# Optimization experiments

Hardware: AMD Instinct MI355X
Metric: run time of the kernel (lower is better)

## Reference

```python
import jax, jax.numpy as jnp
import numpy as np

B, C, D, H, W = 1, 64, 24, 24, 24
N = D * H * W
K = D + H + W - 2  # cross neighbors per node (self deduped)
DS, GD = 64, 64    # d_sim, g_dim
GROUPS = C // 4
EPS = 1e-5
N_ITERS = 2        # pool_strides = [1, 1]


def _build_nbr_idx():
    i, j, k = np.meshgrid(np.arange(D), np.arange(H), np.arange(W), indexing='ij')
    i, j, k = i.reshape(-1), j.reshape(-1), k.reshape(-1)
    a0 = (j * W + k)[:, None] + np.arange(D)[None, :] * (H * W)      # (N, D) full depth line (incl self)
    full1 = (i * H * W + k)[:, None] + np.arange(H)[None, :] * W     # (N, H)
    a1 = full1[np.arange(H)[None, :] != j[:, None]].reshape(N, H - 1)
    full2 = (i * H * W + j * W)[:, None] + np.arange(W)[None, :]     # (N, W)
    a2 = full2[np.arange(W)[None, :] != k[:, None]].reshape(N, W - 1)
    return np.concatenate([a0, a1, a2], axis=1).astype(np.int32)     # (N, K)


def setup_inputs() -> dict:
    key = jax.random.key(0)
    ks = jax.random.split(key, 8)
    s = 0.05
    return {
        'x': jax.random.normal(ks[0], (B, C, D, H, W), jnp.float32),
        'nbr_idx': jnp.asarray(_build_nbr_idx()),
        'phi_w': jax.random.normal(ks[1], (DS, C), jnp.float32) * s,
        'phi_b': jnp.zeros((DS,), jnp.float32),
        'theta_w': jax.random.normal(ks[2], (DS, C), jnp.float32) * s,
        'theta_b': jnp.zeros((DS,), jnp.float32),
        'G_w': jax.random.normal(ks[3], (GD, C), jnp.float32) * s,
        'G_b': jnp.zeros((GD,), jnp.float32),
        'r_w': jax.random.normal(ks[4], (C, GD), jnp.float32) * s,
        'r_b': jnp.zeros((C,), jnp.float32),
        'gn_gamma': jnp.ones((N_ITERS, C), jnp.float32),
        'gn_beta': jnp.zeros((N_ITERS, C), jnp.float32),
        'bn_gamma': jnp.ones((C,), jnp.float32),
        'bn_beta': jnp.zeros((C,), jnp.float32),
        'bn_mean': jnp.zeros((C,), jnp.float32),
        'bn_var': jnp.ones((C,), jnp.float32),
    }


def _group_norm(v, gamma, beta):
    vg = v.reshape(B, GROUPS, C // GROUPS, D, H, W)
    m = vg.mean(axis=(2, 3, 4, 5), keepdims=True)
    var = ((vg - m) ** 2).mean(axis=(2, 3, 4, 5), keepdims=True)
    vn = ((vg - m) / jnp.sqrt(var + EPS)).reshape(B, C, D, H, W)
    return vn * gamma[None, :, None, None, None] + beta[None, :, None, None, None]


def reference(x, nbr_idx, phi_w, phi_b, theta_w, theta_b, G_w, G_b, r_w, r_b,
              gn_gamma, gn_beta, bn_gamma, bn_beta, bn_mean, bn_var):
    h = x
    for it in range(N_ITERS):
        hf = h.reshape(B, C, N).transpose(2, 0, 1)                    # (N, B, C) node features
        theta = jnp.einsum('nbc,dc->nbd', hf, theta_w) + theta_b     # (N, B, DS) queries
        phi_all = jnp.einsum('nbc,dc->nbd', hf, phi_w) + phi_b       # (N, B, DS) keys (pre-gather)
        g_all = jnp.einsum('nbc,gc->nbg', hf, G_w) + G_b             # (N, B, GD) values (pre-gather)
        phi_e = phi_all[nbr_idx]                                      # (N, K, B, DS) mailbox gather
        g_e = g_all[nbr_idx]                                          # (N, K, B, GD)
        f = jnp.einsum('nbd,nkbd->nbk', theta, phi_e)                # attention logits over K
        a = jax.nn.softmax(f, axis=-1)                                # non_local_merge 'softmax'
        y = jnp.einsum('nbk,nkbg->nbg', a, g_e)                      # weighted value sum
        cross = jnp.einsum('nbg,cg->nbc', y, r_w) + r_b              # (N, B, C) output proj
        cross = cross.transpose(1, 2, 0).reshape(B, C, D, H, W)
        h = h + _group_norm(cross, gn_gamma[it], gn_beta[it])
    # BatchNorm3d (eval, running stats) + ReLU
    bc = lambda v: v[None, :, None, None, None]
    out = (h - bc(bn_mean)) / jnp.sqrt(bc(bn_var) + EPS) * bc(bn_gamma) + bc(bn_beta)
    return jax.nn.relu(out)
```

## Files before the change

### kernel.cpp

```cpp
#include <hip/hip_runtime.h>
#include <math.h>

#define NN 13824
#define LW 24

__global__ __launch_bounds__(256) void apply_proj_kernel(
    const float* __restrict__ x,
    const float* __restrict__ cross, const float* __restrict__ gsum,
    const float* __restrict__ gn_g, const float* __restrict__ gn_b,
    float* __restrict__ h_out, int mode,
    const float* __restrict__ theta_w, const float* __restrict__ theta_b,
    const float* __restrict__ phi_w, const float* __restrict__ phi_b,
    const float* __restrict__ g_w, const float* __restrict__ g_b,
    float* __restrict__ tpg)
{
    __shared__ float hs[64 * 64];
    __shared__ float ws[64 * 68];

    const int tid = threadIdx.x;
    const int tile = blockIdx.x / 3, ts = blockIdx.x % 3;
    const int n0 = tile * 64;

    const float* wsel = (ts == 0) ? theta_w : (ts == 1) ? phi_w : g_w;
    const float* bsel = (ts == 0) ? theta_b : (ts == 1) ? phi_b : g_b;

    if (mode == 0) {
        for (int i = tid; i < 4096; i += 256) {
            int c = i >> 6, nl = i & 63;
            hs[c * 64 + nl] = x[(size_t)c * NN + n0 + nl];
        }
    } else {
        for (int i = tid; i < 4096; i += 256) {
            int nl = i >> 6, c = i & 63;
            ws[c * 68 + nl] = cross[(size_t)(n0 + nl) * 64 + c];
        }
        __syncthreads();
        const float inv_cnt = 1.f / 55296.f;
        for (int i = tid; i < 4096; i += 256) {
            int c = i >> 6, nl = i & 63;
            int gr = c >> 2;
            float mean = gsum[gr * 16] * inv_cnt;
            float var = gsum[512 + gr * 16] * inv_cnt - mean * mean;
            float v = (ws[c * 68 + nl] - mean) * rsqrtf(var + 1e-5f) * gn_g[c] + gn_b[c];
            size_t o = (size_t)c * NN + n0 + nl;
            float hv = x[o] + v;
            hs[c * 64 + nl] = hv;
            if (ts == 0) h_out[o] = hv;
        }
        __syncthreads();
    }

    for (int i = tid; i < 4096; i += 256) {
        int d = i >> 6, c = i & 63;
        ws[c * 68 + d] = wsel[d * 64 + c];
    }
    __syncthreads();

    const int d0  = (tid & 15) * 4;
    const int nl0 = (tid >> 4) * 4;
    float acc[4][4];
    #pragma unroll
    for (int q = 0; q < 4; q++)
        #pragma unroll
        for (int j = 0; j < 4; j++) acc[q][j] = 0.f;

    #pragma unroll 4
    for (int c = 0; c < 64; c++) {
        float4 hv = *(const float4*)&hs[c * 64 + nl0];
        float4 wv = *(const float4*)&ws[c * 68 + d0];
        #pragma unroll
        for (int j = 0; j < 4; j++) {
            float w = (&wv.x)[j];
            acc[0][j] += hv.x * w;
            acc[1][j] += hv.y * w;
            acc[2][j] += hv.z * w;
            acc[3][j] += hv.w * w;
        }
    }
    float4 bias = *(const float4*)&bsel[d0];
    #pragma unroll
    for (int q = 0; q < 4; q++) {
        float4 v;
        v.x = acc[q][0] + bias.x; v.y = acc[q][1] + bias.y;
        v.z = acc[q][2] + bias.z; v.w = acc[q][3] + bias.w;
        *(float4*)&tpg[(size_t)(n0 + nl0 + q) * 192 + ts * 64 + d0] = v;
    }
}

__global__ __launch_bounds__(256, 4) void line_attn_kernel(
    const float* __restrict__ tpg,
    float* __restrict__ y_part,
    float* __restrict__ l_part,
    float* __restrict__ gsum)
{
    __shared__ float wbuf[4][2304];

    const int tid = threadIdx.x;
    const int wv = tid >> 6, lane = tid & 63;
    const int line = blockIdx.x * 4 + wv;
    const int axis = line / 576, L = line % 576;
    float* gb = wbuf[wv];
    float* P  = wbuf[wv] + 1632;

    if (blockIdx.x == 0) {
        for (int i = tid; i < 1024; i += 256) gsum[i] = 0.f;
    }

    int base, stride;
    if (axis == 0)      { base = L * 24;                    stride = 1;   }
    else if (axis == 1) { base = (L / 24) * 576 + (L % 24); stride = 24;  }
    else                { base = L;                         stride = 576; }
    const bool excl = (axis != 2);

    float4 gpre[6];
    const int grow = lane >> 4, gquad = lane & 15;
    #pragma unroll
    for (int q = 0; q < 6; q++) {
        int row = q * 4 + grow;
        gpre[q] = *(const float4*)&tpg[(size_t)(base + row * stride) * 192 + 128 + gquad * 4];
    }

    const int li = lane >> 3, lj = lane & 7;
    const int r0 = li * 3, c0 = lj * 3;
    const float* trow[3];
    const float* prow[3];
    #pragma unroll
    for (int a = 0; a < 3; a++) {
        trow[a] = tpg + (size_t)(base + (r0 + a) * stride) * 192;
        prow[a] = tpg + (size_t)(base + (c0 + a) * stride) * 192 + 64;
    }
    float sa[3][3];
    #pragma unroll
    for (int a = 0; a < 3; a++)
        #pragma unroll
        for (int b = 0; b < 3; b++) sa[a][b] = 0.f;
    #pragma unroll 4
    for (int d4 = 0; d4 < 64; d4 += 4) {
        float4 t[3], p[3];
        #pragma unroll
        for (int a = 0; a < 3; a++) t[a] = *(const float4*)&trow[a][d4];
        #pragma unroll
        for (int b = 0; b < 3; b++) p[b] = *(const float4*)&prow[b][d4];
        #pragma unroll
        for (int a = 0; a < 3; a++)
            #pragma unroll
            for (int b = 0; b < 3; b++)
                sa[a][b] += t[a].x * p[b].x + t[a].y * p[b].y +
                            t[a].z * p[b].z + t[a].w * p[b].w;
    }

    float rs[3] = {0.f, 0.f, 0.f};
    #pragma unroll
    for (int a = 0; a < 3; a++)
        #pragma unroll
        for (int b = 0; b < 3; b++) {
            float e = (excl && (r0 + a) == (c0 + b)) ? 0.f : __expf(sa[a][b]);
            rs[a] += e;
            P[(r0 + a) * 28 + c0 + b] = e;
        }
    #pragma unroll
    for (int off = 1; off <= 4; off <<= 1)
        #pragma unroll
        for (int a = 0; a < 3; a++) rs[a] += __shfl_xor(rs[a], off);
    if (lj == 0) {
        #pragma unroll
        for (int a = 0; a < 3; a++)
            l_part[(size_t)axis * NN + base + (r0 + a) * stride] = rs[a];
    }

    #pragma unroll
    for (int q = 0; q < 6; q++)
        *(float4*)&gb[(q * 4 + grow) * 68 + gquad * 4] = gpre[q];
    __threadfence_block();

    const int rg = lane >> 4, dg = lane & 15;
    float acc[6][4];
    #pragma unroll
    for (int i = 0; i < 6; i++)
        #pragma unroll
        for (int k = 0; k < 4; k++) acc[i][k] = 0.f;
    #pragma unroll 4
    for (int c = 0; c < 24; c++) {
        float4 gv = *(const float4*)&gb[c * 68 + dg * 4];
        #pragma unroll
        for (int i = 0; i < 6; i++) {
            float p = P[(rg * 6 + i) * 28 + c];
            acc[i][0] += p * gv.x; acc[i][1] += p * gv.y;
            acc[i][2] += p * gv.z; acc[i][3] += p * gv.w;
        }
    }
    float* yp = y_part + (size_t)axis * NN * 64;
    #pragma unroll
    for (int i = 0; i < 6; i++) {
        float4 v = {acc[i][0], acc[i][1], acc[i][2], acc[i][3]};
        *(float4*)&yp[(size_t)(base + (rg * 6 + i) * stride) * 64 + dg * 4] = v;
    }
}

__global__ __launch_bounds__(256) void combine_kernel(
    const float* __restrict__ y_part, const float* __restrict__ l_part,
    const float* __restrict__ r_w, const float* __restrict__ r_b,
    float* __restrict__ cross, float* __restrict__ gsum)
{
    __shared__ float ys[16 * 68];
    __shared__ float red_s[4][64], red_ss[4][64];

    const int tid = threadIdx.x;
    const int d = tid & 63, w = tid >> 6;
    const int n0 = blockIdx.x * 16;
    const size_t S = (size_t)NN * 64;

    #pragma unroll
    for (int q = 0; q < 4; q++) {
        int nn = w * 4 + q;
        int n = n0 + nn;
        float lv = l_part[n] + l_part[NN + n] + l_part[2 * NN + n];
        size_t o = (size_t)n * 64 + d;
        float yv = y_part[o] + y_part[S + o] + y_part[2 * S + o];
        ys[nn * 68 + d] = yv / lv;
    }
    __syncthreads();

    const int c = d;
    float rb = r_b[c];
    float acc[4] = {rb, rb, rb, rb};
    for (int dd = 0; dd < 64; dd += 4) {
        float4 r4 = *(const float4*)&r_w[c * 64 + dd];
        #pragma unroll
        for (int q = 0; q < 4; q++) {
            float4 y4 = *(const float4*)&ys[(w * 4 + q) * 68 + dd];
            acc[q] += r4.x * y4.x + r4.y * y4.y + r4.z * y4.z + r4.w * y4.w;
        }
    }
    float s = 0.f, ss = 0.f;
    #pragma unroll
    for (int q = 0; q < 4; q++) {
        int n = n0 + w * 4 + q;
        cross[(size_t)n * 64 + c] = acc[q];
        s += acc[q];
        ss += acc[q] * acc[q];
    }
    red_s[w][c] = s;
    red_ss[w][c] = ss;
    __syncthreads();
    if (w == 0) {
        float ts  = red_s[0][c] + red_s[1][c] + red_s[2][c] + red_s[3][c];
        float tss = red_ss[0][c] + red_ss[1][c] + red_ss[2][c] + red_ss[3][c];
        ts  += __shfl_xor(ts, 1);  ts  += __shfl_xor(ts, 2);
        tss += __shfl_xor(tss, 1); tss += __shfl_xor(tss, 2);
        if ((c & 3) == 0) {
            atomicAdd(&gsum[(c >> 2) * 16], ts);
            atomicAdd(&gsum[512 + (c >> 2) * 16], tss);
        }
    }
}

__global__ __launch_bounds__(256) void final_kernel(
    const float* __restrict__ cross,
    const float* __restrict__ gsum,
    const float* __restrict__ gn_g, const float* __restrict__ gn_b,
    const float* __restrict__ h_in,
    const float* __restrict__ bn_g, const float* __restrict__ bn_b,
    const float* __restrict__ bn_m, const float* __restrict__ bn_v,
    float* __restrict__ out)
{
    __shared__ float t[64 * 65];
    const int tid = threadIdx.x;
    const int n0 = blockIdx.x * 64;
    for (int i = tid; i < 4096; i += 256) {
        int nl = i >> 6, c = i & 63;
        t[c * 65 + nl] = cross[(size_t)(n0 + nl) * 64 + c];
    }
    __syncthreads();
    const float inv_cnt = 1.f / 55296.f;
    for (int i = tid; i < 4096; i += 256) {
        int c = i >> 6, nl = i & 63;
        int gr = c >> 2;
        float mean = gsum[gr * 16] * inv_cnt;
        float var = gsum[512 + gr * 16] * inv_cnt - mean * mean;
        float v = (t[c * 65 + nl] - mean) * rsqrtf(var + 1e-5f) * gn_g[c] + gn_b[c];
        size_t o = (size_t)c * NN + n0 + nl;
        float h2 = h_in[o] + v;
        float bnv = (h2 - bn_m[c]) * rsqrtf(bn_v[c] + 1e-5f) * bn_g[c] + bn_b[c];
        out[o] = fmaxf(bnv, 0.f);
    }
}

extern "C" void kernel_launch(void* const* d_in, const int* in_sizes, int n_in,
                              void* d_out, int out_size, void* d_ws, size_t ws_size,
                              hipStream_t stream)
{
    const float* x        = (const float*)d_in[0];
    const float* phi_w    = (const float*)d_in[2];
    const float* phi_b    = (const float*)d_in[3];
    const float* theta_w  = (const float*)d_in[4];
    const float* theta_b  = (const float*)d_in[5];
    const float* G_w      = (const float*)d_in[6];
    const float* G_b      = (const float*)d_in[7];
    const float* r_w      = (const float*)d_in[8];
    const float* r_b      = (const float*)d_in[9];
    const float* gn_gamma = (const float*)d_in[10];
    const float* gn_beta  = (const float*)d_in[11];
    const float* bn_gamma = (const float*)d_in[12];
    const float* bn_beta  = (const float*)d_in[13];
    const float* bn_mean  = (const float*)d_in[14];
    const float* bn_var   = (const float*)d_in[15];

    float* ws = (float*)d_ws;
    const size_t S = (size_t)NN * 64;
    float* h1    = ws;
    float* tpg   = ws + S;
    float* ypart = ws + 4 * S;
    float* cross = ws + 7 * S;
    float* lpart = ws + 8 * S;
    float* gsum  = ws + 8 * S + 3 * NN;

    apply_proj_kernel<<<648, 256, 0, stream>>>(x, cross, gsum, gn_gamma, gn_beta,
                                               h1, 0,
                                               theta_w, theta_b, phi_w, phi_b,
                                               G_w, G_b, tpg);
    line_attn_kernel<<<432, 256, 0, stream>>>(tpg, ypart, lpart, gsum);
    combine_kernel<<<864, 256, 0, stream>>>(ypart, lpart, r_w, r_b, cross, gsum);
    apply_proj_kernel<<<648, 256, 0, stream>>>(x, cross, gsum, gn_gamma, gn_beta,
                                               h1, 1,
                                               theta_w, theta_b, phi_w, phi_b,
                                               G_w, G_b, tpg);
    line_attn_kernel<<<432, 256, 0, stream>>>(tpg, ypart, lpart, gsum);
    combine_kernel<<<864, 256, 0, stream>>>(ypart, lpart, r_w, r_b, cross, gsum);
    final_kernel<<<216, 256, 0, stream>>>(cross, gsum, gn_gamma + 64, gn_beta + 64,
                                          h1, bn_gamma, bn_beta, bn_mean, bn_var,
                                          (float*)d_out);
}
```

Before: 233.0 us.

## Fuse all stages into a persistent kernel with software grid barriers

Replaces the seven separate kernel launches with one persistent kernel of 1024 blocks that runs projection, line attention, combine and final phases in sequence, separated by atomic-counter grid barriers. It also switches many intermediate loads and stores to nontemporal variants and moves GroupNorm statistics into two separately zeroed buffers. The aim is to remove launch gaps and tail effects between stages. The risks are barrier spin overhead, deadlock if not all blocks are co-resident, and poorer cache reuse for nontemporal accesses to freshly written data.

```diff
diff --git a/kernel.cpp b/kernel.cpp
--- a/kernel.cpp
+++ b/kernel.cpp
@@ -2,23 +2,54 @@
 #include <math.h>
 
 #define NN 13824
-#define LW 24
-
-__global__ __launch_bounds__(256) void apply_proj_kernel(
+#define SNODE 884736
+#define GRIDB 1024
+#define INVC (1.0f / 55296.0f)
+
+typedef float floatx4 __attribute__((ext_vector_type(4)));
+
+__device__ __forceinline__ float4 ntl4(const float* p) {
+    floatx4 t = __builtin_nontemporal_load((const floatx4*)p);
+    return make_float4(t.x, t.y, t.z, t.w);
+}
+__device__ __forceinline__ void nts4(float* p, float4 v) {
+    floatx4 t = {v.x, v.y, v.z, v.w};
+    __builtin_nontemporal_store(t, (floatx4*)p);
+}
+__device__ __forceinline__ float ntl1(const float* p) {
+    return __builtin_nontemporal_load(p);
+}
+__device__ __forceinline__ void nts1(float* p, float v) {
+    __builtin_nontemporal_store(v, p);
+}
+
+__device__ __forceinline__ void gbar(unsigned* cnt, unsigned target) {
+    __syncthreads();
+    if (threadIdx.x == 0) {
+        __threadfence();
+        atomicAdd(cnt, 1u);
+        while (__hip_atomic_load(cnt, __ATOMIC_RELAXED, __HIP_MEMORY_SCOPE_AGENT) < target)
+            __builtin_amdgcn_s_sleep(2);
+        __threadfence();
+    }
+    __syncthreads();
+}
+
+__device__ void proj_phase(
+    int b, int mode, float* lds,
     const float* __restrict__ x,
     const float* __restrict__ cross, const float* __restrict__ gsum,
     const float* __restrict__ gn_g, const float* __restrict__ gn_b,
-    float* __restrict__ h_out, int mode,
+    float* __restrict__ h_out,
     const float* __restrict__ theta_w, const float* __restrict__ theta_b,
     const float* __restrict__ phi_w, const float* __restrict__ phi_b,
     const float* __restrict__ g_w, const float* __restrict__ g_b,
     float* __restrict__ tpg)
 {
-    __shared__ float hs[64 * 64];
-    __shared__ float ws[64 * 68];
-
+    float* hs = lds;
+    float* ws = lds + 4096;
     const int tid = threadIdx.x;
-    const int tile = blockIdx.x / 3, ts = blockIdx.x % 3;
+    const int tile = b / 3, ts = b % 3;
     const int n0 = tile * 64;
 
     const float* wsel = (ts == 0) ? theta_w : (ts == 1) ? phi_w : g_w;
@@ -32,20 +63,19 @@
     } else {
         for (int i = tid; i < 4096; i += 256) {
             int nl = i >> 6, c = i & 63;
-            ws[c * 68 + nl] = cross[(size_t)(n0 + nl) * 64 + c];
+            ws[c * 68 + nl] = ntl1(&cross[(size_t)(n0 + nl) * 64 + c]);
         }
         __syncthreads();
-        const float inv_cnt = 1.f / 55296.f;
         for (int i = tid; i < 4096; i += 256) {
             int c = i >> 6, nl = i & 63;
             int gr = c >> 2;
-            float mean = gsum[gr * 16] * inv_cnt;
-            float var = gsum[512 + gr * 16] * inv_cnt - mean * mean;
+            float mean = gsum[gr * 16] * INVC;
+            float var = gsum[512 + gr * 16] * INVC - mean * mean;
             float v = (ws[c * 68 + nl] - mean) * rsqrtf(var + 1e-5f) * gn_g[c] + gn_b[c];
             size_t o = (size_t)c * NN + n0 + nl;
             float hv = x[o] + v;
             hs[c * 64 + nl] = hv;
-            if (ts == 0) h_out[o] = hv;
+            if (ts == 0) nts1(&h_out[o], hv);
         }
         __syncthreads();
     }
@@ -83,41 +113,32 @@
         float4 v;
         v.x = acc[q][0] + bias.x; v.y = acc[q][1] + bias.y;
         v.z = acc[q][2] + bias.z; v.w = acc[q][3] + bias.w;
-        *(float4*)&tpg[(size_t)(n0 + nl0 + q) * 192 + ts * 64 + d0] = v;
-    }
-}
-
-__global__ __launch_bounds__(256, 4) void line_attn_kernel(
+        nts4(&tpg[(size_t)(n0 + nl0 + q) * 192 + ts * 64 + d0], v);
+    }
+    __syncthreads();
+}
+
+__device__ void attn_phase(
+    int line, int lane, float* wlds,
     const float* __restrict__ tpg,
-    float* __restrict__ y_part,
-    float* __restrict__ l_part,
-    float* __restrict__ gsum)
-{
-    __shared__ float wbuf[4][2304];
-
-    const int tid = threadIdx.x;
-    const int wv = tid >> 6, lane = tid & 63;
-    const int line = blockIdx.x * 4 + wv;
+    float* __restrict__ y_part, float* __restrict__ l_part)
+{
+    float* gb = wlds;
+    float* P  = wlds + 1632;
+
     const int axis = line / 576, L = line % 576;
-    float* gb = wbuf[wv];
-    float* P  = wbuf[wv] + 1632;
-
-    if (blockIdx.x == 0) {
-        for (int i = tid; i < 1024; i += 256) gsum[i] = 0.f;
-    }
-
     int base, stride;
     if (axis == 0)      { base = L * 24;                    stride = 1;   }
     else if (axis == 1) { base = (L / 24) * 576 + (L % 24); stride = 24;  }
     else                { base = L;                         stride = 576; }
     const bool excl = (axis != 2);
 
-    float4 gpre[6];
-    const int grow = lane >> 4, gquad = lane & 15;
+    const int grow = lane >> 4, gq = (lane & 15) * 4;
     #pragma unroll
     for (int q = 0; q < 6; q++) {
         int row = q * 4 + grow;
-        gpre[q] = *(const float4*)&tpg[(size_t)(base + row * stride) * 192 + 128 + gquad * 4];
+        float4 gv = *(const float4*)&tpg[(size_t)(base + row * stride) * 192 + 128 + gq];
+        *(float4*)&gb[row * 68 + gq] = gv;
     }
 
     const int li = lane >> 3, lj = lane & 7;
@@ -165,12 +186,8 @@
     if (lj == 0) {
         #pragma unroll
         for (int a = 0; a < 3; a++)
-            l_part[(size_t)axis * NN + base + (r0 + a) * stride] = rs[a];
-    }
-
-    #pragma unroll
-    for (int q = 0; q < 6; q++)
-        *(float4*)&gb[(q * 4 + grow) * 68 + gquad * 4] = gpre[q];
+            nts1(&l_part[(size_t)axis * NN + base + (r0 + a) * stride], rs[a]);
+    }
     __threadfence_block();
 
     const int rg = lane >> 4, dg = lane & 15;
@@ -189,34 +206,34 @@
             acc[i][2] += p * gv.z; acc[i][3] += p * gv.w;
         }
     }
-    float* yp = y_part + (size_t)axis * NN * 64;
+    float* yp = y_part + (size_t)axis * SNODE;
     #pragma unroll
     for (int i = 0; i < 6; i++) {
         float4 v = {acc[i][0], acc[i][1], acc[i][2], acc[i][3]};
-        *(float4*)&yp[(size_t)(base + (rg * 6 + i) * stride) * 64 + dg * 4] = v;
-    }
-}
-
-__global__ __launch_bounds__(256) void combine_kernel(
+        nts4(&yp[(size_t)(base + (rg * 6 + i) * stride) * 64 + dg * 4], v);
+    }
+}
+
+__device__ void combine_phase(
+    int b, float* lds,
     const float* __restrict__ y_part, const float* __restrict__ l_part,
     const float* __restrict__ r_w, const float* __restrict__ r_b,
     float* __restrict__ cross, float* __restrict__ gsum)
 {
-    __shared__ float ys[16 * 68];
-    __shared__ float red_s[4][64], red_ss[4][64];
-
+    float* ys     = lds;
+    float* red_s  = lds + 1088;
+    float* red_ss = lds + 1344;
     const int tid = threadIdx.x;
     const int d = tid & 63, w = tid >> 6;
-    const int n0 = blockIdx.x * 16;
-    const size_t S = (size_t)NN * 64;
+    const int n0 = b * 16;
 
     #pragma unroll
     for (int q = 0; q < 4; q++) {
         int nn = w * 4 + q;
         int n = n0 + nn;
-        float lv = l_part[n] + l_part[NN + n] + l_part[2 * NN + n];
+        float lv = ntl1(&l_part[n]) + ntl1(&l_part[NN + n]) + ntl1(&l_part[2 * NN + n]);
         size_t o = (size_t)n * 64 + d;
-        float yv = y_part[o] + y_part[S + o] + y_part[2 * S + o];
+        float yv = ntl1(&y_part[o]) + ntl1(&y_part[SNODE + o]) + ntl1(&y_part[2 * SNODE + o]);
         ys[nn * 68 + d] = yv / lv;
     }
     __syncthreads();
@@ -236,16 +253,16 @@
     #pragma unroll
     for (int q = 0; q < 4; q++) {
         int n = n0 + w * 4 + q;
-        cross[(size_t)n * 64 + c] = acc[q];
+        nts1(&cross[(size_t)n * 64 + c], acc[q]);
         s += acc[q];
         ss += acc[q] * acc[q];
     }
-    red_s[w][c] = s;
-    red_ss[w][c] = ss;
+    red_s[w * 64 + c] = s;
+    red_ss[w * 64 + c] = ss;
     __syncthreads();
     if (w == 0) {
-        float ts  = red_s[0][c] + red_s[1][c] + red_s[2][c] + red_s[3][c];
-        float tss = red_ss[0][c] + red_ss[1][c] + red_ss[2][c] + red_ss[3][c];
+        float ts  = red_s[c] + red_s[64 + c] + red_s[128 + c] + red_s[192 + c];
+        float tss = red_ss[c] + red_ss[64 + c] + red_ss[128 + c] + red_ss[192 + c];
         ts  += __shfl_xor(ts, 1);  ts  += __shfl_xor(ts, 2);
         tss += __shfl_xor(tss, 1); tss += __shfl_xor(tss, 2);
         if ((c & 3) == 0) {
@@ -253,37 +270,88 @@
             atomicAdd(&gsum[512 + (c >> 2) * 16], tss);
         }
     }
-}
-
-__global__ __launch_bounds__(256) void final_kernel(
-    const float* __restrict__ cross,
-    const float* __restrict__ gsum,
+    __syncthreads();
+}
+
+__device__ void final_phase(
+    int b, float* lds,
+    const float* __restrict__ cross, const float* __restrict__ gsum,
     const float* __restrict__ gn_g, const float* __restrict__ gn_b,
     const float* __restrict__ h_in,
     const float* __restrict__ bn_g, const float* __restrict__ bn_b,
     const float* __restrict__ bn_m, const float* __restrict__ bn_v,
     float* __restrict__ out)
 {
-    __shared__ float t[64 * 65];
+    float* t = lds;
     const int tid = threadIdx.x;
-    const int n0 = blockIdx.x * 64;
+    const int n0 = b * 64;
     for (int i = tid; i < 4096; i += 256) {
         int nl = i >> 6, c = i & 63;
-        t[c * 65 + nl] = cross[(size_t)(n0 + nl) * 64 + c];
-    }
-    __syncthreads();
-    const float inv_cnt = 1.f / 55296.f;
+        t[c * 65 + nl] = ntl1(&cross[(size_t)(n0 + nl) * 64 + c]);
+    }
+    __syncthreads();
     for (int i = tid; i < 4096; i += 256) {
         int c = i >> 6, nl = i & 63;
         int gr = c >> 2;
-        float mean = gsum[gr * 16] * inv_cnt;
-        float var = gsum[512 + gr * 16] * inv_cnt - mean * mean;
+        float mean = gsum[gr * 16] * INVC;
+        float var = gsum[512 + gr * 16] * INVC - mean * mean;
         float v = (t[c * 65 + nl] - mean) * rsqrtf(var + 1e-5f) * gn_g[c] + gn_b[c];
         size_t o = (size_t)c * NN + n0 + nl;
-        float h2 = h_in[o] + v;
+        float h2 = ntl1(&h_in[o]) + v;
         float bnv = (h2 - bn_m[c]) * rsqrtf(bn_v[c] + 1e-5f) * bn_g[c] + bn_b[c];
         out[o] = fmaxf(bnv, 0.f);
     }
+}
+
+__global__ __launch_bounds__(256) void zero_kernel(float* g, unsigned* cnt) {
+    int t = blockIdx.x * 256 + threadIdx.x;
+    g[t] = 0.f;
+    if (t == 0) *cnt = 0u;
+}
+
+__global__ __launch_bounds__(256, 4) void mega_kernel(
+    const float* __restrict__ x,
+    const float* __restrict__ theta_w, const float* __restrict__ theta_b,
+    const float* __restrict__ phi_w,   const float* __restrict__ phi_b,
+    const float* __restrict__ g_w,     const float* __restrict__ g_b,
+    const float* __restrict__ r_w,     const float* __restrict__ r_b,
+    const float* __restrict__ gn_g,    const float* __restrict__ gn_b,
+    const float* __restrict__ bn_g,    const float* __restrict__ bn_b,
+    const float* __restrict__ bn_m,    const float* __restrict__ bn_v,
+    float* __restrict__ tpg, float* __restrict__ ypart, float* __restrict__ lpart,
+    float* __restrict__ h1, float* __restrict__ cross,
+    float* __restrict__ gsumA, float* __restrict__ gsumB,
+    unsigned* __restrict__ cnt, float* __restrict__ out)
+{
+    __shared__ float lds[9216];
+    const int b = blockIdx.x, tid = threadIdx.x;
+    const int wv = tid >> 6, lane = tid & 63;
+
+    if (b < 648)
+        proj_phase(b, 0, lds, x, cross, gsumA, gn_g, gn_b, h1,
+                   theta_w, theta_b, phi_w, phi_b, g_w, g_b, tpg);
+    gbar(cnt, 1 * GRIDB);
+
+    { int line = b * 4 + wv; if (line < 1728) attn_phase(line, lane, lds + wv * 2304, tpg, ypart, lpart); }
+    gbar(cnt, 2 * GRIDB);
+
+    if (b < 864) combine_phase(b, lds, ypart, lpart, r_w, r_b, cross, gsumA);
+    gbar(cnt, 3 * GRIDB);
+
+    if (b < 648)
+        proj_phase(b, 1, lds, x, cross, gsumA, gn_g, gn_b, h1,
+                   theta_w, theta_b, phi_w, phi_b, g_w, g_b, tpg);
+    gbar(cnt, 4 * GRIDB);
+
+    { int line = b * 4 + wv; if (line < 1728) attn_phase(line, lane, lds + wv * 2304, tpg, ypart, lpart); }
+    gbar(cnt, 5 * GRIDB);
+
+    if (b < 864) combine_phase(b, lds, ypart, lpart, r_w, r_b, cross, gsumB);
+    gbar(cnt, 6 * GRIDB);
+
+    if (b < 216)
+        final_phase(b, lds, cross, gsumB, gn_g + 64, gn_b + 64, h1,
+                    bn_g, bn_b, bn_m, bn_v, out);
 }
 
 extern "C" void kernel_launch(void* const* d_in, const int* in_sizes, int n_in,
@@ -307,27 +375,18 @@
     const float* bn_var   = (const float*)d_in[15];
 
     float* ws = (float*)d_ws;
-    const size_t S = (size_t)NN * 64;
-    float* h1    = ws;
-    float* tpg   = ws + S;
-    float* ypart = ws + 4 * S;
-    float* cross = ws + 7 * S;
-    float* lpart = ws + 8 * S;
-    float* gsum  = ws + 8 * S + 3 * NN;
-
-    apply_proj_kernel<<<648, 256, 0, stream>>>(x, cross, gsum, gn_gamma, gn_beta,
-                                               h1, 0,
-                                               theta_w, theta_b, phi_w, phi_b,
-                                               G_w, G_b, tpg);
-    line_attn_kernel<<<432, 256, 0, stream>>>(tpg, ypart, lpart, gsum);
-    combine_kernel<<<864, 256, 0, stream>>>(ypart, lpart, r_w, r_b, cross, gsum);
-    apply_proj_kernel<<<648, 256, 0, stream>>>(x, cross, gsum, gn_gamma, gn_beta,
-                                               h1, 1,
-                                               theta_w, theta_b, phi_w, phi_b,
-                                               G_w, G_b, tpg);
-    line_attn_kernel<<<432, 256, 0, stream>>>(tpg, ypart, lpart, gsum);
-    combine_kernel<<<864, 256, 0, stream>>>(ypart, lpart, r_w, r_b, cross, gsum);
-    final_kernel<<<216, 256, 0, stream>>>(cross, gsum, gn_gamma + 64, gn_beta + 64,
-                                          h1, bn_gamma, bn_beta, bn_mean, bn_var,
-                                          (float*)d_out);
-}
+    float* tpg   = ws;
+    float* ypart = ws + 2654208;
+    float* h1    = ws + 5308416;
+    float* cross = ws + 6193152;
+    float* lpart = ws + 7077888;
+    float* gsumA = ws + 7119360;
+    float* gsumB = ws + 7120384;
+    unsigned* cnt = (unsigned*)(ws + 7121408);
+
+    zero_kernel<<<8, 256, 0, stream>>>(gsumA, cnt);
+    mega_kernel<<<GRIDB, 256, 0, stream>>>(
+        x, theta_w, theta_b, phi_w, phi_b, G_w, G_b, r_w, r_b,
+        gn_gamma, gn_beta, bn_gamma, bn_beta, bn_mean, bn_var,
+        tpg, ypart, lpart, h1, cross, gsumA, gsumB, cnt, (float*)d_out);
+}
```

Result: slower. 922.1 us (+295.7%).

## Split line attention across two waves per line along feature dimension

Applied to the files above, without the earlier changes.

Each line is now handled by two wavefronts that each take half of the 64-wide feature dimension. Both waves compute partial logits that are summed through shared memory, and each wave then produces half of the weighted value output. The grid doubles to 864 blocks, which raises parallelism and cuts per-thread register and latency cost. In exchange it adds block-wide barriers, an extra shared-memory round trip for the logits, and duplicated exp/softmax work in both halves.

```diff
diff --git a/kernel.cpp b/kernel.cpp
--- a/kernel.cpp
+++ b/kernel.cpp
@@ -87,20 +87,23 @@
     }
 }
 
-__global__ __launch_bounds__(256, 4) void line_attn_kernel(
+__global__ __launch_bounds__(256) void line_attn_kernel(
     const float* __restrict__ tpg,
     float* __restrict__ y_part,
     float* __restrict__ l_part,
     float* __restrict__ gsum)
 {
-    __shared__ float wbuf[4][2304];
+    __shared__ float lds[2][3584];
 
     const int tid = threadIdx.x;
     const int wv = tid >> 6, lane = tid & 63;
-    const int line = blockIdx.x * 4 + wv;
+    const int ll = wv >> 1, hf = wv & 1;
+    const int line = blockIdx.x * 2 + ll;
     const int axis = line / 576, L = line % 576;
-    float* gb = wbuf[wv];
-    float* P  = wbuf[wv] + 1632;
+
+    float* Sp = lds[ll];
+    float* P  = lds[ll] + 1152;
+    float* gb = lds[ll] + 1824 + hf * 880;
 
     if (blockIdx.x == 0) {
         for (int i = tid; i < 1024; i += 256) gsum[i] = 0.f;
@@ -111,13 +114,14 @@
     else if (axis == 1) { base = (L / 24) * 576 + (L % 24); stride = 24;  }
     else                { base = L;                         stride = 576; }
     const bool excl = (axis != 2);
-
-    float4 gpre[6];
-    const int grow = lane >> 4, gquad = lane & 15;
-    #pragma unroll
-    for (int q = 0; q < 6; q++) {
-        int row = q * 4 + grow;
-        gpre[q] = *(const float4*)&tpg[(size_t)(base + row * stride) * 192 + 128 + gquad * 4];
+    const int d0h = hf * 32;
+
+    #pragma unroll
+    for (int q = 0; q < 3; q++) {
+        int idx = q * 64 + lane;
+        int row = idx >> 3, dq = (idx & 7) * 4;
+        float4 gv = *(const float4*)&tpg[(size_t)(base + row * stride) * 192 + 128 + d0h + dq];
+        *(float4*)&gb[row * 36 + dq] = gv;
     }
 
     const int li = lane >> 3, lj = lane & 7;
@@ -126,16 +130,16 @@
     const float* prow[3];
     #pragma unroll
     for (int a = 0; a < 3; a++) {
-        trow[a] = tpg + (size_t)(base + (r0 + a) * stride) * 192;
-        prow[a] = tpg + (size_t)(base + (c0 + a) * stride) * 192 + 64;
+        trow[a] = tpg + (size_t)(base + (r0 + a) * stride) * 192 + d0h;
+        prow[a] = tpg + (size_t)(base + (c0 + a) * stride) * 192 + 64 + d0h;
     }
     float sa[3][3];
     #pragma unroll
     for (int a = 0; a < 3; a++)
         #pragma unroll
         for (int b = 0; b < 3; b++) sa[a][b] = 0.f;
-    #pragma unroll 4
-    for (int d4 = 0; d4 < 64; d4 += 4) {
+    #pragma unroll 8
+    for (int d4 = 0; d4 < 32; d4 += 4) {
         float4 t[3], p[3];
         #pragma unroll
         for (int a = 0; a < 3; a++) t[a] = *(const float4*)&trow[a][d4];
@@ -148,13 +152,21 @@
                 sa[a][b] += t[a].x * p[b].x + t[a].y * p[b].y +
                             t[a].z * p[b].z + t[a].w * p[b].w;
     }
+    #pragma unroll
+    for (int a = 0; a < 3; a++)
+        #pragma unroll
+        for (int b = 0; b < 3; b++)
+            Sp[hf * 576 + (r0 + a) * 24 + c0 + b] = sa[a][b];
+    __syncthreads();
 
     float rs[3] = {0.f, 0.f, 0.f};
     #pragma unroll
     for (int a = 0; a < 3; a++)
         #pragma unroll
         for (int b = 0; b < 3; b++) {
-            float e = (excl && (r0 + a) == (c0 + b)) ? 0.f : __expf(sa[a][b]);
+            int e0 = (r0 + a) * 24 + c0 + b;
+            float s = Sp[e0] + Sp[576 + e0];
+            float e = (excl && (r0 + a) == (c0 + b)) ? 0.f : __expf(s);
             rs[a] += e;
             P[(r0 + a) * 28 + c0 + b] = e;
         }
@@ -162,38 +174,34 @@
     for (int off = 1; off <= 4; off <<= 1)
         #pragma unroll
         for (int a = 0; a < 3; a++) rs[a] += __shfl_xor(rs[a], off);
-    if (lj == 0) {
+    if (hf == 0 && lj == 0) {
         #pragma unroll
         for (int a = 0; a < 3; a++)
             l_part[(size_t)axis * NN + base + (r0 + a) * stride] = rs[a];
     }
-
-    #pragma unroll
-    for (int q = 0; q < 6; q++)
-        *(float4*)&gb[(q * 4 + grow) * 68 + gquad * 4] = gpre[q];
-    __threadfence_block();
-
-    const int rg = lane >> 4, dg = lane & 15;
-    float acc[6][4];
-    #pragma unroll
-    for (int i = 0; i < 6; i++)
+    __syncthreads();
+
+    const int rg = lane >> 3, dq8 = lane & 7;
+    float acc[3][4];
+    #pragma unroll
+    for (int i = 0; i < 3; i++)
         #pragma unroll
         for (int k = 0; k < 4; k++) acc[i][k] = 0.f;
     #pragma unroll 4
     for (int c = 0; c < 24; c++) {
-        float4 gv = *(const float4*)&gb[c * 68 + dg * 4];
-        #pragma unroll
-        for (int i = 0; i < 6; i++) {
-            float p = P[(rg * 6 + i) * 28 + c];
+        float4 gv = *(const float4*)&gb[c * 36 + dq8 * 4];
+        #pragma unroll
+        for (int i = 0; i < 3; i++) {
+            float p = P[(rg * 3 + i) * 28 + c];
             acc[i][0] += p * gv.x; acc[i][1] += p * gv.y;
             acc[i][2] += p * gv.z; acc[i][3] += p * gv.w;
         }
     }
     float* yp = y_part + (size_t)axis * NN * 64;
     #pragma unroll
-    for (int i = 0; i < 6; i++) {
+    for (int i = 0; i < 3; i++) {
         float4 v = {acc[i][0], acc[i][1], acc[i][2], acc[i][3]};
-        *(float4*)&yp[(size_t)(base + (rg * 6 + i) * stride) * 64 + dg * 4] = v;
+        *(float4*)&yp[(size_t)(base + (rg * 3 + i) * stride) * 64 + d0h + dq8 * 4] = v;
     }
 }
 
@@ -319,13 +327,13 @@
                                                h1, 0,
                                                theta_w, theta_b, phi_w, phi_b,
                                                G_w, G_b, tpg);
-    line_attn_kernel<<<432, 256, 0, stream>>>(tpg, ypart, lpart, gsum);
+    line_attn_kernel<<<864, 256, 0, stream>>>(tpg, ypart, lpart, gsum);
     combine_kernel<<<864, 256, 0, stream>>>(ypart, lpart, r_w, r_b, cross, gsum);
     apply_proj_kernel<<<648, 256, 0, stream>>>(x, cross, gsum, gn_gamma, gn_beta,
                                                h1, 1,
                                                theta_w, theta_b, phi_w, phi_b,
                                                G_w, G_b, tpg);
-    line_attn_kernel<<<432, 256, 0, stream>>>(tpg, ypart, lpart, gsum);
+    line_attn_kernel<<<864, 256, 0, stream>>>(tpg, ypart, lpart, gsum);
     combine_kernel<<<864, 256, 0, stream>>>(ypart, lpart, r_w, r_b, cross, gsum);
     final_kernel<<<216, 256, 0, stream>>>(cross, gsum, gn_gamma + 64, gn_beta + 64,
                                           h1, bn_gamma, bn_beta, bn_mean, bn_var,
```

Measured after the change: 230.4 us. Within noise of the previous version (-1.1%).
